# Kernel tuning notes

Measured on AMD Instinct MI355X. Metric: run time of the kernel, lower is better.

The kernel has to match this reference:

```python
import jax, jax.numpy as jnp
import numpy as np

N, E, G = 100_000, 1_600_000, 64
NODE_DIM, EDGE_DIM = 64, 16
H, C = 4, 16            # heads, per-head channels (hidden_dim=64)
HID = H * C             # 64
OUT = 128
NEG_SLOPE = 0.2


def _gatv2(x, src, dst, ea, Wl, bl, Wr, br, We, att, bias, n):
    """One GATv2Conv layer (PyG semantics, concat=True). src/dst include self-loops."""
    xl = (x @ Wl + bl).reshape(-1, H, C)   # [n,H,C] source transform
    xr = (x @ Wr + br).reshape(-1, H, C)   # [n,H,C] target transform
    e = (ea @ We).reshape(-1, H, C)        # [E2,H,C] edge transform (no bias)
    m = jax.nn.leaky_relu(xl[src] + xr[dst] + e, NEG_SLOPE)  # [E2,H,C]
    score = jnp.einsum('ehc,hc->eh', m, att)                 # [E2,H]
    smax = jax.ops.segment_max(score, dst, num_segments=n)   # scatter-softmax over dst
    z = jnp.exp(score - smax[dst])
    denom = jax.ops.segment_sum(z, dst, num_segments=n)
    alpha = z / denom[dst]                                   # [E2,H]
    out = jax.ops.segment_sum(alpha[..., None] * xl[src], dst, num_segments=n)
    return out.reshape(n, HID) + bias


def setup_inputs() -> dict:
    key = jax.random.key(0)
    ks = jax.random.split(key, 24)
    inp = {
        'node_features': jax.random.normal(ks[0], (N, NODE_DIM), jnp.float32),
        'edge_index': jax.random.randint(ks[1], (2, E), 0, N),
        'edge_attr': jax.random.normal(ks[2], (E, EDGE_DIM), jnp.float32),
        'batch': jnp.sort(jax.random.randint(ks[3], (N,), 0, G)),
    }
    s = 0.1
    i = 4
    for l, ind in (('l0', NODE_DIM), ('l1', HID)):
        inp[f'{l}_Wl'] = jax.random.normal(ks[i], (ind, HID), jnp.float32) * s; i += 1
        inp[f'{l}_bl'] = jnp.zeros((HID,), jnp.float32)
        inp[f'{l}_Wr'] = jax.random.normal(ks[i], (ind, HID), jnp.float32) * s; i += 1
        inp[f'{l}_br'] = jnp.zeros((HID,), jnp.float32)
        inp[f'{l}_We'] = jax.random.normal(ks[i], (EDGE_DIM, HID), jnp.float32) * s; i += 1
        inp[f'{l}_att'] = jax.random.normal(ks[i], (H, C), jnp.float32) * s; i += 1
        inp[f'{l}_bias'] = jnp.zeros((HID,), jnp.float32)
    inp['mlp_W1'] = jax.random.normal(ks[i], (HID, OUT), jnp.float32) * s; i += 1
    inp['mlp_b1'] = jnp.zeros((OUT,), jnp.float32)
    inp['mlp_W2'] = jax.random.normal(ks[i], (OUT, OUT), jnp.float32) * s
    inp['mlp_b2'] = jnp.zeros((OUT,), jnp.float32)
    return inp


def reference(node_features, edge_index, edge_attr, batch,
              l0_Wl, l0_bl, l0_Wr, l0_br, l0_We, l0_att, l0_bias,
              l1_Wl, l1_bl, l1_Wr, l1_br, l1_We, l1_att, l1_bias,
              mlp_W1, mlp_b1, mlp_W2, mlp_b2):
    n = node_features.shape[0]
    src, dst = edge_index[0], edge_index[1]
    # add_self_loops with fill_value='mean': self-loop attr = mean of incoming edge attrs
    cnt = jax.ops.segment_sum(jnp.ones((edge_attr.shape[0],), edge_attr.dtype), dst, num_segments=n)
    loop_attr = jax.ops.segment_sum(edge_attr, dst, num_segments=n) / jnp.maximum(cnt, 1.0)[:, None]
    loop = jnp.arange(n)
    src2 = jnp.concatenate([src, loop])
    dst2 = jnp.concatenate([dst, loop])
    ea2 = jnp.concatenate([edge_attr, loop_attr], axis=0)

    x = jax.nn.relu(_gatv2(node_features, src2, dst2, ea2,
                           l0_Wl, l0_bl, l0_Wr, l0_br, l0_We, l0_att, l0_bias, n))
    x = jax.nn.relu(_gatv2(x, src2, dst2, ea2,
                           l1_Wl, l1_bl, l1_Wr, l1_br, l1_We, l1_att, l1_bias, n))

    # global_mean_pool
    gcnt = jax.ops.segment_sum(jnp.ones((n,), x.dtype), batch, num_segments=G)
    g = jax.ops.segment_sum(x, batch, num_segments=G) / jnp.maximum(gcnt, 1.0)[:, None]

    return jax.nn.relu(g @ mlp_W1 + mlp_b1) @ mlp_W2 + mlp_b2
```

## Files before the change

kernel.cpp:

```cpp
#include <hip/hip_runtime.h>
#include <math.h>

#define HID 64
#define NH 4
#define NC 16
#define EDIM 16
#define OUTD 128
#define NEG 0.2f

typedef float v4f __attribute__((ext_vector_type(4)));
typedef float v2f __attribute__((ext_vector_type(2)));

__device__ __forceinline__ v2f pkfma(v2f a, v2f b, v2f c) {
    return __builtin_elementwise_fma(a, b, c);
}

template <int CTRL>
__device__ __forceinline__ float dpp_add(float x) {
    int t = __builtin_amdgcn_update_dpp(0, __float_as_int(x), CTRL, 0xF, 0xF, true);
    return x + __int_as_float(t);
}
__device__ __forceinline__ float red16(float x) {
    x = dpp_add<0xB1>(x);
    x = dpp_add<0x4E>(x);
    x = dpp_add<0x124>(x);
    x = dpp_add<0x128>(x);
    return x;
}



__global__ void hist_kernel(const int* __restrict__ dst, int* __restrict__ deg,
                            int* __restrict__ rank, int E) {
    int e = blockIdx.x * 256 + threadIdx.x;
    if (e < E) rank[e] = atomicAdd(&deg[dst[e]], 1);
}

__global__ void scan_a(const int* __restrict__ deg, int* __restrict__ offs,
                       int* __restrict__ bsum, int n) {
    __shared__ int tmp[1024];
    int i = blockIdx.x * 1024 + threadIdx.x;
    int v = (i < n) ? (deg[i] + 1) : 0;
    tmp[threadIdx.x] = v;
    __syncthreads();
    for (int off = 1; off < 1024; off <<= 1) {
        int t = (threadIdx.x >= off) ? tmp[threadIdx.x - off] : 0;
        __syncthreads();
        tmp[threadIdx.x] += t;
        __syncthreads();
    }
    if (i < n) offs[i] = tmp[threadIdx.x] - v;
    if (threadIdx.x == 1023) bsum[blockIdx.x] = tmp[1023];
}

__global__ void scan_b(int* __restrict__ bsum, int* __restrict__ offs, int nb, int n) {
    __shared__ int tmp[1024];
    int v = (threadIdx.x < nb) ? bsum[threadIdx.x] : 0;
    tmp[threadIdx.x] = v;
    __syncthreads();
    for (int off = 1; off < 1024; off <<= 1) {
        int t = (threadIdx.x >= off) ? tmp[threadIdx.x - off] : 0;
        __syncthreads();
        tmp[threadIdx.x] += t;
        __syncthreads();
    }
    if (threadIdx.x < nb) bsum[threadIdx.x] = tmp[threadIdx.x] - v;
    if (threadIdx.x == 1023) offs[n] = tmp[1023];
}

__global__ void scan_c(int* __restrict__ offs, const int* __restrict__ bsum, int n) {
    int i = blockIdx.x * 1024 + threadIdx.x;
    if (i < n) offs[i] += bsum[blockIdx.x];
}

__global__ void scatter_kernel(const int* __restrict__ src, const int* __restrict__ dst,
                               const int* __restrict__ rank,
                               const v4f* __restrict__ ea,
                               const int* __restrict__ offs,
                               int* __restrict__ csr_src, v4f* __restrict__ csr_ea,
                               int E) {
    int e = blockIdx.x * 256 + threadIdx.x;
    if (e >= E) return;
    int d = dst[e];
    int p = offs[d] + 1 + rank[e];
    csr_src[p] = src[e];
    v4f a0 = ea[e * 4 + 0], a1 = ea[e * 4 + 1],
        a2 = ea[e * 4 + 2], a3 = ea[e * 4 + 3];
    csr_ea[p * 4 + 0] = a0;
    csr_ea[p * 4 + 1] = a1;
    csr_ea[p * 4 + 2] = a2;
    csr_ea[p * 4 + 3] = a3;
}

__global__ void loopattr_kernel(const int* __restrict__ offs, int* __restrict__ csr_src,
                                float* __restrict__ csr_ea_f, int n) {
    int idx = blockIdx.x * 256 + threadIdx.x;
    if (idx >= n * EDIM) return;
    int nd = idx >> 4, k = idx & 15;
    int e0 = offs[nd], e1 = offs[nd + 1];
    int deg = e1 - e0 - 1;
    float s = 0.f;
    for (int j = e0 + 1; j < e1; j++) s += csr_ea_f[(size_t)j * EDIM + k];
    csr_ea_f[(size_t)e0 * EDIM + k] = s / fmaxf((float)deg, 1.0f);
    if (k == 0) csr_src[e0] = nd;
}


__global__ __launch_bounds__(256)
void dualgemm_kernel(const float* __restrict__ x,
                     const float* __restrict__ Wl, const float* __restrict__ bl,
                     const float* __restrict__ Wr, const float* __restrict__ br,
                     float* __restrict__ xl, float* __restrict__ xr, int n) {
    __shared__ float xs[64 * 65];
    __shared__ float ws[64 * 128];
    int tid = threadIdx.x;
    int r0 = blockIdx.x * 64;

#pragma unroll
    for (int t = 0; t < 32; t++) {
        int idx = t * 256 + tid;
        int k = idx >> 7, j = idx & 127;
        ws[idx] = (j < 64) ? Wl[k * 64 + j] : Wr[k * 64 + (j - 64)];
    }
#pragma unroll
    for (int t = 0; t < 16; t++) {
        int idx = t * 256 + tid;
        int r = idx >> 6, c = idx & 63;
        float v = (r0 + r < n) ? x[(r0 + r) * 64 + c] : 0.f;
        xs[r * 65 + c] = v;
    }
    __syncthreads();

    int cg = tid & 31;
    int rg = tid >> 5;

    float acc[8][4];
#pragma unroll
    for (int u = 0; u < 8; u++)
#pragma unroll
        for (int v = 0; v < 4; v++) acc[u][v] = 0.f;

    for (int k = 0; k < 64; k++) {
        float4 wv = *(const float4*)&ws[k * 128 + cg * 4];
        float xv[8];
#pragma unroll
        for (int u = 0; u < 8; u++) xv[u] = xs[(rg * 8 + u) * 65 + k];
#pragma unroll
        for (int u = 0; u < 8; u++) {
            acc[u][0] += xv[u] * wv.x;
            acc[u][1] += xv[u] * wv.y;
            acc[u][2] += xv[u] * wv.z;
            acc[u][3] += xv[u] * wv.w;
        }
    }

    int j0 = cg * 4;
    bool isL = (j0 < 64);
    const float* bp = isL ? bl : br;
    float* op = isL ? xl : xr;
    int jj = isL ? j0 : (j0 - 64);
    float4 bv = *(const float4*)&bp[jj];
#pragma unroll
    for (int u = 0; u < 8; u++) {
        int r = r0 + rg * 8 + u;
        if (r < n) {
            float4 o;
            o.x = acc[u][0] + bv.x; o.y = acc[u][1] + bv.y;
            o.z = acc[u][2] + bv.z; o.w = acc[u][3] + bv.w;
            *(float4*)&op[r * 64 + jj] = o;
        }
    }
}


#define EDOT(A0, A1, A2, A3, INIT)                                         \
    ({ v2f _a = {(INIT), 0.f};                                             \
       _a = pkfma((v2f){A0.x, A0.y}, wec2[0], _a);                         \
       _a = pkfma((v2f){A0.z, A0.w}, wec2[1], _a);                         \
       _a = pkfma((v2f){A1.x, A1.y}, wec2[2], _a);                         \
       _a = pkfma((v2f){A1.z, A1.w}, wec2[3], _a);                         \
       _a = pkfma((v2f){A2.x, A2.y}, wec2[4], _a);                         \
       _a = pkfma((v2f){A2.z, A2.w}, wec2[5], _a);                         \
       _a = pkfma((v2f){A3.x, A3.y}, wec2[6], _a);                         \
       _a = pkfma((v2f){A3.z, A3.w}, wec2[7], _a);                         \
       _a.x + _a.y; })

#define LOADS(K, BI) do { int _s = base + 2 * (K);                         \
    sb##BI##0 = csr_src[_s]; sb##BI##1 = csr_src[_s + 1]; } while (0)
#define LOADA(K, BI) do { int _q = (base + 2 * (K)) * 4;                   \
    ab##BI##0 = csr_ea[_q + 0]; ab##BI##1 = csr_ea[_q + 1];                \
    ab##BI##2 = csr_ea[_q + 2]; ab##BI##3 = csr_ea[_q + 3];                \
    ab##BI##4 = csr_ea[_q + 4]; ab##BI##5 = csr_ea[_q + 5];                \
    ab##BI##6 = csr_ea[_q + 6]; ab##BI##7 = csr_ea[_q + 7]; } while (0)
#define GATH(BI) do {                                                      \
    xa##BI = (xl + (size_t)sb##BI##0 * 64)[lane];                          \
    xc##BI = (xl + (size_t)sb##BI##1 * 64)[lane]; } while (0)
#define COMP(BI) do {                                                      \
    float m0 = EDOT(ab##BI##0, ab##BI##1, ab##BI##2, ab##BI##3, xa##BI + xrl); \
    float m1 = EDOT(ab##BI##4, ab##BI##5, ab##BI##6, ab##BI##7, xc##BI + xrl); \
    m0 = fmaxf(m0, NEG * m0);                                              \
    m1 = fmaxf(m1, NEG * m1);                                              \
    float p0 = red16(m0 * attl);                                           \
    float p1 = red16(m1 * attl);                                           \
    float z0 = __builtin_amdgcn_exp2f(p0);                                 \
    float z1 = __builtin_amdgcn_exp2f(p1);                                 \
    S += z0 + z1;                                                          \
    acc = fmaf(z0, xa##BI, fmaf(z1, xc##BI, acc)); } while (0)
#define PHASE(P, Q) do {                                                   \
    int _k2 = t + 2; _k2 = (_k2 > lastp) ? lastp : _k2;                    \
    int _k3 = t + 3; _k3 = (_k3 > lastp) ? lastp : _k3;                    \
    GATH(Q);                                                               \
    LOADA(_k2, Q);                                                         \
    LOADS(_k3, P);                                                         \
    COMP(P); } while (0)

__global__ __launch_bounds__(256)
void gat_kernel(const int* __restrict__ offs, const int* __restrict__ csr_src,
                const float4* __restrict__ csr_ea,
                const float* __restrict__ xl, const float* __restrict__ xr,
                const float* __restrict__ We, const float* __restrict__ att,
                const float* __restrict__ bias, float* __restrict__ out, int n) {
    int lane = threadIdx.x & 63;
    int node = __builtin_amdgcn_readfirstlane(blockIdx.x * 4 + (threadIdx.x >> 6));
    if (node >= n) return;

    v2f wec2[8];
#pragma unroll
    for (int k = 0; k < 8; k++) {
        wec2[k].x = We[(2 * k) * 64 + lane];
        wec2[k].y = We[(2 * k + 1) * 64 + lane];
    }
    const float LOG2E = 1.4426950408889634f;
    float attl = att[lane] * LOG2E;
    float xrl = xr[(size_t)node * 64 + lane];

    int e0 = __builtin_amdgcn_readfirstlane(offs[node]);
    int e1 = __builtin_amdgcn_readfirstlane(offs[node + 1]);

    float S = 0.f, acc = 0.f;
    int i = e0;

    if ((e1 - e0) & 1) {
        int s0 = csr_src[i];
        float4 A0 = csr_ea[i*4+0], A1 = csr_ea[i*4+1],
               A2 = csr_ea[i*4+2], A3 = csr_ea[i*4+3];
        float x0 = (xl + (size_t)s0 * 64)[lane];
        float m0 = EDOT(A0, A1, A2, A3, x0 + xrl);
        m0 = fmaxf(m0, NEG * m0);
        float p0 = red16(m0 * attl);
        float z0 = __builtin_amdgcn_exp2f(p0);
        S = z0; acc = z0 * x0;
        i++;
    }

    if (i < e1) {
        int base = i;
        int lastp = ((e1 - i) >> 1) - 1;
        int sb00, sb01, sb10, sb11, sb20, sb21;
        float4 ab00, ab01, ab02, ab03, ab04, ab05, ab06, ab07;
        float4 ab10, ab11, ab12, ab13, ab14, ab15, ab16, ab17;
        float4 ab20, ab21, ab22, ab23, ab24, ab25, ab26, ab27;
        float xa0, xc0, xa1, xc1, xa2, xc2;

        int k1 = (1 > lastp) ? lastp : 1;
        int k2 = (2 > lastp) ? lastp : 2;
        LOADS(0, 0); LOADS(k1, 1); LOADS(k2, 2);
        LOADA(0, 0); LOADA(k1, 1);
        GATH(0); GATH(1);

        int t = 0;
        for (;;) {
            PHASE(0, 2); if (t >= lastp) break; ++t;
            PHASE(1, 0); if (t >= lastp) break; ++t;
            PHASE(2, 1); if (t >= lastp) break; ++t;
        }
    }
    out[(size_t)node * 64 + lane] = fmaxf(acc / S + bias[lane], 0.f);
}


__global__ __launch_bounds__(256)
void pool_mlp_kernel(const float* __restrict__ x, const int* __restrict__ batch, int n,
                     const float* __restrict__ W1, const float* __restrict__ b1,
                     const float* __restrict__ W2, const float* __restrict__ b2,
                     float* __restrict__ out) {
    __shared__ float psum[4][64];
    __shared__ float gv[64];
    __shared__ float hid[128];
    __shared__ int bounds[2];

    int g = blockIdx.x;
    int tid = threadIdx.x;
    int wave = tid >> 6, lane = tid & 63;

    if (tid < 2) {
        int target = g + tid;
        int lo = 0, hi = n;
        while (lo < hi) {
            int mid = (lo + hi) >> 1;
            if (batch[mid] < target) lo = mid + 1; else hi = mid;
        }
        bounds[tid] = lo;
    }
    __syncthreads();
    int lo = bounds[0], hi = bounds[1];
    int cnt = hi - lo;

    float s = 0.f;
    for (int nd = lo + wave; nd < hi; nd += 4)
        s += x[(size_t)nd * 64 + lane];
    psum[wave][lane] = s;
    __syncthreads();

    if (tid < 64)
        gv[tid] = (psum[0][tid] + psum[1][tid] + psum[2][tid] + psum[3][tid])
                  / fmaxf((float)cnt, 1.0f);
    __syncthreads();

    if (tid < 128) {
        float h = b1[tid];
        for (int k = 0; k < 64; k++) h += gv[k] * W1[k * 128 + tid];
        hid[tid] = fmaxf(h, 0.f);
    }
    __syncthreads();
    if (tid < 128) {
        float o = b2[tid];
        for (int k = 0; k < 128; k++) o += hid[k] * W2[k * 128 + tid];
        out[g * 128 + tid] = o;
    }
}


extern "C" void kernel_launch(void* const* d_in, const int* in_sizes, int n_in,
                              void* d_out, int out_size, void* d_ws, size_t ws_size,
                              hipStream_t stream) {
    const float* nf   = (const float*)d_in[0];
    const int*   ei   = (const int*)d_in[1];
    const float* eaw  = (const float*)d_in[2];
    const int*   bat  = (const int*)d_in[3];
    const float* l0_Wl = (const float*)d_in[4];
    const float* l0_bl = (const float*)d_in[5];
    const float* l0_Wr = (const float*)d_in[6];
    const float* l0_br = (const float*)d_in[7];
    const float* l0_We = (const float*)d_in[8];
    const float* l0_att = (const float*)d_in[9];
    const float* l0_bias = (const float*)d_in[10];
    const float* l1_Wl = (const float*)d_in[11];
    const float* l1_bl = (const float*)d_in[12];
    const float* l1_Wr = (const float*)d_in[13];
    const float* l1_br = (const float*)d_in[14];
    const float* l1_We = (const float*)d_in[15];
    const float* l1_att = (const float*)d_in[16];
    const float* l1_bias = (const float*)d_in[17];
    const float* mW1 = (const float*)d_in[18];
    const float* mb1 = (const float*)d_in[19];
    const float* mW2 = (const float*)d_in[20];
    const float* mb2 = (const float*)d_in[21];

    const int N = in_sizes[0] / 64;
    const int E = in_sizes[1] / 2;
    const int G = out_size / OUTD;

    char* w = (char*)d_ws;
    auto carve = [&](size_t bytes) {
        void* p = (void*)w;
        w += (bytes + 255) & ~(size_t)255;
        return p;
    };
    int*    deg     = (int*)carve((size_t)N * 4);
    int*    offs    = (int*)carve((size_t)(N + 1) * 4);
    int*    rank    = (int*)carve((size_t)E * 4);
    int*    bsum    = (int*)carve(4096 * 4);
    int*    csr_src = (int*)carve((size_t)(E + N) * 4);
    v4f*    csr_ea  = (v4f*)carve((size_t)(E + N) * 64);
    float*  xl      = (float*)carve((size_t)N * 64 * 4);
    float*  xr      = (float*)carve((size_t)N * 64 * 4);
    float*  x1      = (float*)carve((size_t)N * 64 * 4);

    hipMemsetAsync(deg, 0, (size_t)N * 4, stream);

    const int* src = ei;
    const int* dst = ei + E;

    hist_kernel<<<(E + 255) / 256, 256, 0, stream>>>(dst, deg, rank, E);

    int nb = (N + 1023) / 1024;
    scan_a<<<nb, 1024, 0, stream>>>(deg, offs, bsum, N);
    scan_b<<<1, 1024, 0, stream>>>(bsum, offs, nb, N);
    scan_c<<<nb, 1024, 0, stream>>>(offs, bsum, N);

    scatter_kernel<<<(E + 255) / 256, 256, 0, stream>>>(src, dst, rank, (const v4f*)eaw,
                                                        offs, csr_src, csr_ea, E);
    loopattr_kernel<<<(N * EDIM + 255) / 256, 256, 0, stream>>>(offs, csr_src,
                                                                (float*)csr_ea, N);

    dualgemm_kernel<<<(N + 63) / 64, 256, 0, stream>>>(nf, l0_Wl, l0_bl, l0_Wr, l0_br,
                                                       xl, xr, N);
    gat_kernel<<<(N + 3) / 4, 256, 0, stream>>>(offs, csr_src, (const float4*)csr_ea,
                                                xl, xr, l0_We, l0_att, l0_bias, x1, N);
    dualgemm_kernel<<<(N + 63) / 64, 256, 0, stream>>>(x1, l1_Wl, l1_bl, l1_Wr, l1_br,
                                                       xl, xr, N);
    gat_kernel<<<(N + 3) / 4, 256, 0, stream>>>(offs, csr_src, (const float4*)csr_ea,
                                                xl, xr, l1_We, l1_att, l1_bias, x1, N);

    pool_mlp_kernel<<<G, 256, 0, stream>>>(x1, bat, N, mW1, mb1, mW2, mb2, (float*)d_out);
}
```

Baseline: 803.6 us.

## Replace CSR edge-attribute copy with indirect (src, edge-id) records

The scatter no longer copies each 64-byte edge attribute row into CSR order. It writes an int2 record holding the source node and the original edge id, and self-loop attributes go to a separate small array. Loopattr and both GAT layers then gather attributes indirectly through the edge id, choosing between the original array and the loop array. This removes a large scattered write of about 100 MB in setup. The cost is random, non-contiguous attribute reads in every GAT pass, a dependent load chain (record, then attribute) and a per-edge branch in the prefetch pipeline.

```diff
diff --git a/kernel.cpp b/kernel.cpp
--- a/kernel.cpp
+++ b/kernel.cpp
@@ -75,34 +75,30 @@
 
 __global__ void scatter_kernel(const int* __restrict__ src, const int* __restrict__ dst,
                                const int* __restrict__ rank,
-                               const v4f* __restrict__ ea,
                                const int* __restrict__ offs,
-                               int* __restrict__ csr_src, v4f* __restrict__ csr_ea,
-                               int E) {
+                               int2* __restrict__ csr_rec, int E) {
     int e = blockIdx.x * 256 + threadIdx.x;
     if (e >= E) return;
     int d = dst[e];
     int p = offs[d] + 1 + rank[e];
-    csr_src[p] = src[e];
-    v4f a0 = ea[e * 4 + 0], a1 = ea[e * 4 + 1],
-        a2 = ea[e * 4 + 2], a3 = ea[e * 4 + 3];
-    csr_ea[p * 4 + 0] = a0;
-    csr_ea[p * 4 + 1] = a1;
-    csr_ea[p * 4 + 2] = a2;
-    csr_ea[p * 4 + 3] = a3;
-}
-
-__global__ void loopattr_kernel(const int* __restrict__ offs, int* __restrict__ csr_src,
-                                float* __restrict__ csr_ea_f, int n) {
+    csr_rec[p] = make_int2(src[e], e);
+}
+
+__global__ void loopattr_kernel(const int* __restrict__ offs, int2* __restrict__ csr_rec,
+                                const float* __restrict__ ea, float* __restrict__ la,
+                                int n, int E) {
     int idx = blockIdx.x * 256 + threadIdx.x;
     if (idx >= n * EDIM) return;
     int nd = idx >> 4, k = idx & 15;
     int e0 = offs[nd], e1 = offs[nd + 1];
     int deg = e1 - e0 - 1;
     float s = 0.f;
-    for (int j = e0 + 1; j < e1; j++) s += csr_ea_f[(size_t)j * EDIM + k];
-    csr_ea_f[(size_t)e0 * EDIM + k] = s / fmaxf((float)deg, 1.0f);
-    if (k == 0) csr_src[e0] = nd;
+    for (int j = e0 + 1; j < e1; j++) {
+        int eid = csr_rec[j].y;
+        s += ea[(size_t)eid * EDIM + k];
+    }
+    la[(size_t)nd * EDIM + k] = s / fmaxf((float)deg, 1.0f);
+    if (k == 0) csr_rec[e0] = make_int2(nd, E + nd);
 }
 
 
@@ -185,13 +181,20 @@
        _a = pkfma((v2f){A3.z, A3.w}, wec2[7], _a);                         \
        _a.x + _a.y; })
 
+#define ATTRP(EID) ((EID) < E ? ea4 + (size_t)(EID) * 4                    \
+                              : la4 + (size_t)((EID) - E) * 4)
+
 #define LOADS(K, BI) do { int _s = base + 2 * (K);                         \
-    sb##BI##0 = csr_src[_s]; sb##BI##1 = csr_src[_s + 1]; } while (0)
-#define LOADA(K, BI) do { int _q = (base + 2 * (K)) * 4;                   \
-    ab##BI##0 = csr_ea[_q + 0]; ab##BI##1 = csr_ea[_q + 1];                \
-    ab##BI##2 = csr_ea[_q + 2]; ab##BI##3 = csr_ea[_q + 3];                \
-    ab##BI##4 = csr_ea[_q + 4]; ab##BI##5 = csr_ea[_q + 5];                \
-    ab##BI##6 = csr_ea[_q + 6]; ab##BI##7 = csr_ea[_q + 7]; } while (0)
+    int2 _r0 = csr_rec[_s], _r1 = csr_rec[_s + 1];                         \
+    sb##BI##0 = _r0.x; eb##BI##0 = _r0.y;                                  \
+    sb##BI##1 = _r1.x; eb##BI##1 = _r1.y; } while (0)
+#define LOADA(BI) do {                                                     \
+    const float4* _pa = ATTRP(eb##BI##0);                                  \
+    const float4* _pb = ATTRP(eb##BI##1);                                  \
+    ab##BI##0 = _pa[0]; ab##BI##1 = _pa[1];                                \
+    ab##BI##2 = _pa[2]; ab##BI##3 = _pa[3];                                \
+    ab##BI##4 = _pb[0]; ab##BI##5 = _pb[1];                                \
+    ab##BI##6 = _pb[2]; ab##BI##7 = _pb[3]; } while (0)
 #define GATH(BI) do {                                                      \
     xa##BI = (xl + (size_t)sb##BI##0 * 64)[lane];                          \
     xc##BI = (xl + (size_t)sb##BI##1 * 64)[lane]; } while (0)
@@ -207,23 +210,26 @@
     S += z0 + z1;                                                          \
     acc = fmaf(z0, xa##BI, fmaf(z1, xc##BI, acc)); } while (0)
 #define PHASE(P, Q) do {                                                   \
-    int _k2 = t + 2; _k2 = (_k2 > lastp) ? lastp : _k2;                    \
     int _k3 = t + 3; _k3 = (_k3 > lastp) ? lastp : _k3;                    \
     GATH(Q);                                                               \
-    LOADA(_k2, Q);                                                         \
+    LOADA(Q);                                                              \
     LOADS(_k3, P);                                                         \
     COMP(P); } while (0)
 
 __global__ __launch_bounds__(256)
-void gat_kernel(const int* __restrict__ offs, const int* __restrict__ csr_src,
-                const float4* __restrict__ csr_ea,
+void gat_kernel(const int* __restrict__ offs, const int2* __restrict__ csr_rec,
+                const float* __restrict__ ea, const float* __restrict__ la,
                 const float* __restrict__ xl, const float* __restrict__ xr,
                 const float* __restrict__ We, const float* __restrict__ att,
-                const float* __restrict__ bias, float* __restrict__ out, int n) {
+                const float* __restrict__ bias, float* __restrict__ out,
+                int n, int E) {
     int lane = threadIdx.x & 63;
     int node = __builtin_amdgcn_readfirstlane(blockIdx.x * 4 + (threadIdx.x >> 6));
     if (node >= n) return;
 
+    const float4* ea4 = (const float4*)ea;
+    const float4* la4 = (const float4*)la;
+
     v2f wec2[8];
 #pragma unroll
     for (int k = 0; k < 8; k++) {
@@ -241,9 +247,10 @@
     int i = e0;
 
     if ((e1 - e0) & 1) {
-        int s0 = csr_src[i];
-        float4 A0 = csr_ea[i*4+0], A1 = csr_ea[i*4+1],
-               A2 = csr_ea[i*4+2], A3 = csr_ea[i*4+3];
+        int2 r = csr_rec[i];
+        int s0 = r.x;
+        const float4* ap = ATTRP(r.y);
+        float4 A0 = ap[0], A1 = ap[1], A2 = ap[2], A3 = ap[3];
         float x0 = (xl + (size_t)s0 * 64)[lane];
         float m0 = EDOT(A0, A1, A2, A3, x0 + xrl);
         m0 = fmaxf(m0, NEG * m0);
@@ -257,6 +264,7 @@
         int base = i;
         int lastp = ((e1 - i) >> 1) - 1;
         int sb00, sb01, sb10, sb11, sb20, sb21;
+        int eb00, eb01, eb10, eb11, eb20, eb21;
         float4 ab00, ab01, ab02, ab03, ab04, ab05, ab06, ab07;
         float4 ab10, ab11, ab12, ab13, ab14, ab15, ab16, ab17;
         float4 ab20, ab21, ab22, ab23, ab24, ab25, ab26, ab27;
@@ -265,7 +273,7 @@
         int k1 = (1 > lastp) ? lastp : 1;
         int k2 = (2 > lastp) ? lastp : 2;
         LOADS(0, 0); LOADS(k1, 1); LOADS(k2, 2);
-        LOADA(0, 0); LOADA(k1, 1);
+        LOADA(0); LOADA(1);
         GATH(0); GATH(1);
 
         int t = 0;
@@ -371,8 +379,8 @@
     int*    offs    = (int*)carve((size_t)(N + 1) * 4);
     int*    rank    = (int*)carve((size_t)E * 4);
     int*    bsum    = (int*)carve(4096 * 4);
-    int*    csr_src = (int*)carve((size_t)(E + N) * 4);
-    v4f*    csr_ea  = (v4f*)carve((size_t)(E + N) * 64);
+    int2*   csr_rec = (int2*)carve((size_t)(E + N) * 8);
+    float*  la      = (float*)carve((size_t)N * EDIM * 4);
     float*  xl      = (float*)carve((size_t)N * 64 * 4);
     float*  xr      = (float*)carve((size_t)N * 64 * 4);
     float*  x1      = (float*)carve((size_t)N * 64 * 4);
@@ -389,19 +397,19 @@
     scan_b<<<1, 1024, 0, stream>>>(bsum, offs, nb, N);
     scan_c<<<nb, 1024, 0, stream>>>(offs, bsum, N);
 
-    scatter_kernel<<<(E + 255) / 256, 256, 0, stream>>>(src, dst, rank, (const v4f*)eaw,
-                                                        offs, csr_src, csr_ea, E);
-    loopattr_kernel<<<(N * EDIM + 255) / 256, 256, 0, stream>>>(offs, csr_src,
-                                                                (float*)csr_ea, N);
+    scatter_kernel<<<(E + 255) / 256, 256, 0, stream>>>(src, dst, rank, offs,
+                                                        csr_rec, E);
+    loopattr_kernel<<<(N * EDIM + 255) / 256, 256, 0, stream>>>(offs, csr_rec,
+                                                                eaw, la, N, E);
 
     dualgemm_kernel<<<(N + 63) / 64, 256, 0, stream>>>(nf, l0_Wl, l0_bl, l0_Wr, l0_br,
                                                        xl, xr, N);
-    gat_kernel<<<(N + 3) / 4, 256, 0, stream>>>(offs, csr_src, (const float4*)csr_ea,
-                                                xl, xr, l0_We, l0_att, l0_bias, x1, N);
+    gat_kernel<<<(N + 3) / 4, 256, 0, stream>>>(offs, csr_rec, eaw, la, xl, xr,
+                                                l0_We, l0_att, l0_bias, x1, N, E);
     dualgemm_kernel<<<(N + 63) / 64, 256, 0, stream>>>(x1, l1_Wl, l1_bl, l1_Wr, l1_br,
                                                        xl, xr, N);
-    gat_kernel<<<(N + 3) / 4, 256, 0, stream>>>(offs, csr_src, (const float4*)csr_ea,
-                                                xl, xr, l1_We, l1_att, l1_bias, x1, N);
+    gat_kernel<<<(N + 3) / 4, 256, 0, stream>>>(offs, csr_rec, eaw, la, xl, xr,
+                                                l1_We, l1_att, l1_bias, x1, N, E);
 
     pool_mlp_kernel<<<G, 256, 0, stream>>>(x1, bat, N, mW1, mb1, mW2, mb2, (float*)d_out);
 }
```

Result: faster. 774.1 us (-3.7%).
